# Optimization experiments

Hardware: AMD Instinct MI355X
Metric: run time of the kernel (lower is better)

Reference implementation:

```python
import jax, jax.numpy as jnp
import numpy as np

DELTA_V = 0.1
DELTA_D = 0.5
NUM_LABELS = 33  # label 0 = background, instance ids 1..32


def setup_inputs() -> dict:
    key = jax.random.key(0)
    k1, k2 = jax.random.split(key)
    B, N, D = 8, 131072, 32
    embeddings = jax.random.normal(k1, (B, N, D), dtype=jnp.float32)
    labels = jax.random.randint(k2, (B, N), 0, NUM_LABELS, dtype=jnp.int32)
    return {"embeddings": embeddings, "labels": labels}


def reference(embeddings, labels):
    # embeddings: [B, N, D], labels: [B, N] int (0 = ignore)
    B = embeddings.shape[0]
    dt = embeddings.dtype

    oh = jax.nn.one_hot(labels, NUM_LABELS, dtype=dt)              # [B, N, L]
    counts = oh.sum(1)                                              # [B, L]
    sums = jnp.einsum('bnl,bnd->bld', oh, embeddings)               # [B, L, D]
    means = sums / jnp.maximum(counts, 1.0)[..., None]              # [B, L, D]

    # ---- pull loss: hinge on distance of each point to its instance mean ----
    mean_pt = jnp.take_along_axis(means, labels[..., None], axis=1)  # [B, N, D]
    diff = embeddings - mean_pt
    dist = jnp.sqrt(jnp.sum(diff * diff, -1) + 1e-24)               # [B, N]
    hinge = jnp.maximum(dist - DELTA_V, 0.0)
    seg_mean = jnp.einsum('bnl,bn->bl', oh, hinge) / jnp.maximum(counts, 1.0)  # [B, L]

    present = counts[:, 1:] > 0                                     # [B, L-1]
    n_inst = present.sum(-1).astype(dt)                             # [B]
    pull_b = seg_mean[:, 1:].sum(-1) / (n_inst + 1e-6)
    pull = pull_b.sum() / B

    # ---- push loss: hinge margin between normalized instance means ----
    m = means[:, 1:, :]                                             # [B, L-1, D]
    mn = m / jnp.maximum(jnp.linalg.norm(m, axis=-1, keepdims=True), 1e-12)
    sq = jnp.sum((mn[:, :, None, :] - mn[:, None, :, :]) ** 2, -1)  # [B, K, K]
    dmat = jnp.sqrt(sq + 1e-24)
    K = NUM_LABELS - 1
    triu = jnp.triu(jnp.ones((K, K), dt), 1)
    pmask = triu[None] * present[:, :, None].astype(dt) * present[:, None, :].astype(dt)
    hp = jnp.maximum(2.0 * DELTA_D - dmat, 0.0) * pmask
    push_b = jnp.where(n_inst > 1, hp.sum((-2, -1)) / (pmask.sum((-2, -1)) + 1e-6), 0.0)
    push = push_b.sum() / B

    total = pull + push
    return jnp.stack([total, pull, push])
```

## Files before the change

kernel.cpp:

```cpp
#include <hip/hip_runtime.h>
#include <hip/hip_bf16.h>

#define BATCH 8
#define NPTS  131072
#define DIM   32
#define NLAB  33
#define G1X   128
#define P1PTS 1024
#define BPB2  512

#define OFF_CNT   0
#define OFF_SUM   264
#define OFF_PULL  (264 + 8448)
#define WS_FLOATS (OFF_PULL + 8)

typedef short  bf16x8 __attribute__((ext_vector_type(8)));
typedef float  f32x4  __attribute__((ext_vector_type(4)));

static __device__ __forceinline__ short f2bf(float f) {
  __hip_bfloat16 h = __float2bfloat16(f);
  return *reinterpret_cast<short*>(&h);
}

__global__ __launch_bounds__(256) void pass1_kernel(
    const float* __restrict__ emb, const int* __restrict__ lab,
    float* __restrict__ gsum, float* __restrict__ gcnt) {
  const int b    = blockIdx.y;
  const int tid  = threadIdx.x;
  const int w    = tid >> 6;
  const int lane = tid & 63;

  __shared__ float s_stage[4][32 * 33];
  __shared__ int   s_cnt4[4][NLAB];
  float* st = s_stage[w];

  const size_t base = (size_t)b * NPTS + (size_t)blockIdx.x * P1PTS + w * 256;

  const int m0 = lane & 15;
  const int g  = lane >> 4;
  f32x4 acc[3][2];
#pragma unroll
  for (int t = 0; t < 3; ++t)
#pragma unroll
    for (int u = 0; u < 2; ++u) acc[t][u] = (f32x4){0.f, 0.f, 0.f, 0.f};
  int cnt0 = 0, cnt1 = 0, cnt2 = 0;

  float4 ld[4];
  int labv;
  {
    const float4* src = (const float4*)(emb + base * DIM);
#pragma unroll
    for (int r = 0; r < 4; ++r) ld[r] = src[lane + 64 * r];
    labv = lab[base + (lane & 31)];
  }

  for (int step = 0; step < 8; ++step) {
#pragma unroll
    for (int r = 0; r < 4; ++r) {
      const int i = lane + 64 * r;
      const int p = i >> 3, d0 = (i & 7) * 4;
      st[(d0 + 0) * 33 + p] = ld[r].x;
      st[(d0 + 1) * 33 + p] = ld[r].y;
      st[(d0 + 2) * 33 + p] = ld[r].z;
      st[(d0 + 3) * 33 + p] = ld[r].w;
    }
    const int labv_c = labv;

    if (step < 7) {
      const float4* src = (const float4*)(emb + (base + (step + 1) * 32) * DIM);
#pragma unroll
      for (int r = 0; r < 4; ++r) ld[r] = src[lane + 64 * r];
      labv = lab[base + (step + 1) * 32 + (lane & 31)];
    }

    bf16x8 a0, a1, a2;
#pragma unroll
    for (int j = 0; j < 8; ++j) {
      const int lj = __shfl(labv_c, g * 8 + j);
      const int h0 = (lj == m0), h1 = (lj == m0 + 16), h2 = (lj == m0 + 32);
      a0[j] = h0 ? (short)0x3F80 : (short)0;
      a1[j] = h1 ? (short)0x3F80 : (short)0;
      a2[j] = h2 ? (short)0x3F80 : (short)0;
      cnt0 += h0; cnt1 += h1; cnt2 += h2;
    }

    bf16x8 b0, b1;
#pragma unroll
    for (int j = 0; j < 8; ++j) {
      b0[j] = f2bf(st[m0 * 33 + g * 8 + j]);
      b1[j] = f2bf(st[(m0 + 16) * 33 + g * 8 + j]);
    }

    acc[0][0] = __builtin_amdgcn_mfma_f32_16x16x32_bf16(a0, b0, acc[0][0], 0, 0, 0);
    acc[0][1] = __builtin_amdgcn_mfma_f32_16x16x32_bf16(a0, b1, acc[0][1], 0, 0, 0);
    acc[1][0] = __builtin_amdgcn_mfma_f32_16x16x32_bf16(a1, b0, acc[1][0], 0, 0, 0);
    acc[1][1] = __builtin_amdgcn_mfma_f32_16x16x32_bf16(a1, b1, acc[1][1], 0, 0, 0);
    acc[2][0] = __builtin_amdgcn_mfma_f32_16x16x32_bf16(a2, b0, acc[2][0], 0, 0, 0);
    acc[2][1] = __builtin_amdgcn_mfma_f32_16x16x32_bf16(a2, b1, acc[2][1], 0, 0, 0);
  }

  cnt0 += __shfl_xor(cnt0, 16); cnt0 += __shfl_xor(cnt0, 32);
  cnt1 += __shfl_xor(cnt1, 16); cnt1 += __shfl_xor(cnt1, 32);
  cnt2 += __shfl_xor(cnt2, 16); cnt2 += __shfl_xor(cnt2, 32);
  if (lane < 16)            s_cnt4[w][m0]      = cnt0;
  else if (lane < 32)       s_cnt4[w][m0 + 16] = cnt1;
  if (lane == 32)           s_cnt4[w][32]      = cnt2;

#pragma unroll
  for (int t = 0; t < 2; ++t)
#pragma unroll
    for (int u = 0; u < 2; ++u)
#pragma unroll
      for (int r = 0; r < 4; ++r)
        st[(t * 16 + g * 4 + r) * DIM + m0 + 16 * u] = acc[t][u][r];
  if (lane < 16) {
    st[32 * DIM + m0]      = acc[2][0][0];
    st[32 * DIM + m0 + 16] = acc[2][1][0];
  }
  __syncthreads();

  for (int i = tid; i < NLAB * DIM; i += 256) {
    const float v = s_stage[0][i] + s_stage[1][i] + s_stage[2][i] + s_stage[3][i];
    atomicAdd(&gsum[(size_t)b * (NLAB * DIM) + i], v);
  }
  if (tid < NLAB) {
    const int c = s_cnt4[0][tid] + s_cnt4[1][tid] + s_cnt4[2][tid] + s_cnt4[3][tid];
    atomicAdd(&gcnt[b * NLAB + tid], (float)c);
  }
}

__global__ __launch_bounds__(256) void pass2_kernel(
    const float* __restrict__ emb, const int* __restrict__ lab,
    const float* __restrict__ gsum, const float* __restrict__ gcnt,
    float* __restrict__ pullb) {
  const int b   = blockIdx.y;
  const int tid = threadIdx.x;
  __shared__ __align__(16) float s_mean[NLAB * 36];
  __shared__ float s_w[NLAB];
  __shared__ float s_red[4];

  for (int i = tid; i < NLAB * DIM; i += 256) {
    const int l = i >> 5, d = i & 31;
    const float c = gcnt[b * NLAB + l];
    s_mean[l * 36 + d] = gsum[b * (NLAB * DIM) + i] / fmaxf(c, 1.0f);
  }
  if (tid < 64) {
    const float c = (tid < NLAB) ? gcnt[b * NLAB + tid] : 0.f;
    const int pres = (tid >= 1 && tid < NLAB && c > 0.f) ? 1 : 0;
    const unsigned long long bal = __ballot(pres);
    const float n_inst = (float)__popcll(bal);
    if (tid < NLAB)
      s_w[tid] = pres ? 1.f / (fmaxf(c, 1.f) * (n_inst + 1e-6f)) : 0.f;
  }
  __syncthreads();

  const int sub   = tid >> 3;
  const int lane8 = tid & 7;
  const int d0    = lane8 << 2;
  const size_t base = (size_t)b * NPTS;
  const int p0 = blockIdx.x * 32 + sub;
  constexpr int NIT = NPTS / (BPB2 * 32);

  int labs[NIT];
#pragma unroll
  for (int it = 0; it < NIT; ++it)
    labs[it] = lab[base + p0 + it * (BPB2 * 32)];

  float wacc = 0.f;
#pragma unroll
  for (int it = 0; it < NIT; ++it) {
    const int p = p0 + it * (BPB2 * 32);
    const int l = labs[it];
    const float4 e = *(const float4*)(emb + (base + p) * DIM + d0);
    const float4 m = *(const float4*)(s_mean + l * 36 + d0);
    const float dx = e.x - m.x, dy = e.y - m.y, dz = e.z - m.z, dw = e.w - m.w;
    float s = dx * dx + dy * dy + dz * dz + dw * dw;
    s += __shfl_xor(s, 1);
    s += __shfl_xor(s, 2);
    s += __shfl_xor(s, 4);
    if (lane8 == 0) {
      const float dist = sqrtf(s + 1e-24f);
      wacc += s_w[l] * fmaxf(dist - 0.1f, 0.f);
    }
  }
#pragma unroll
  for (int m = 1; m < 64; m <<= 1) wacc += __shfl_xor(wacc, m);
  if ((tid & 63) == 0) s_red[tid >> 6] = wacc;
  __syncthreads();
  if (tid == 0)
    atomicAdd(&pullb[b], s_red[0] + s_red[1] + s_red[2] + s_red[3]);
}

__global__ __launch_bounds__(512) void finish_kernel(
    const float* __restrict__ gsum, const float* __restrict__ gcnt,
    const float* __restrict__ pullb, float* __restrict__ out) {
  const int tid = threadIdx.x;
  const int b   = tid >> 6;
  const int t   = tid & 63;
  __shared__ __align__(16) float s_mn[BATCH * 32 * DIM];
  __shared__ float s_ps[BATCH];
  float* mn = s_mn + b * 32 * DIM;

  int pres = 0;
  if (t < 32) {
    const int l = t + 1;
    const float cnt = gcnt[b * NLAB + l];
    pres = (cnt > 0.f) ? 1 : 0;
    const float inv = 1.f / fmaxf(cnt, 1.f);
    float v[DIM];
    float n2 = 0.f;
    for (int d = 0; d < DIM; d++) {
      v[d] = gsum[b * (NLAB * DIM) + l * DIM + d] * inv;
      n2  += v[d] * v[d];
    }
    const float scale = 1.f / fmaxf(sqrtf(n2), 1e-12f);
    for (int d = 0; d < DIM; d++) mn[t * DIM + d] = v[d] * scale;
  }
  const unsigned long long bal = __ballot(pres);
  const unsigned int pmask32 = (unsigned int)(bal & 0xFFFFFFFFull);
  const int n_inst = __popc(pmask32);

  __syncthreads();

  float hp_sum = 0.f, pm_sum = 0.f;
  for (int idx = t; idx < 1024; idx += 64) {
    const int i = idx >> 5, j = idx & 31;
    if (j > i && ((pmask32 >> i) & 1u) && ((pmask32 >> j) & 1u)) {
      const float4* a = (const float4*)(mn + i * DIM);
      const float4* c = (const float4*)(mn + j * DIM);
      float sq = 0.f;
      for (int q = 0; q < 8; q++) {
        const float4 av = a[q], cv = c[q];
        const float dx = av.x - cv.x, dy = av.y - cv.y;
        const float dz = av.z - cv.z, dw = av.w - cv.w;
        sq += dx * dx + dy * dy + dz * dz + dw * dw;
      }
      const float dmat = sqrtf(sq + 1e-24f);
      hp_sum += fmaxf(1.0f - dmat, 0.f);
      pm_sum += 1.f;
    }
  }
  for (int m = 1; m < 64; m <<= 1) {
    hp_sum += __shfl_xor(hp_sum, m);
    pm_sum += __shfl_xor(pm_sum, m);
  }
  const float push = (n_inst > 1) ? hp_sum / (pm_sum + 1e-6f) : 0.f;
  if (t == 0) s_ps[b] = push;
  __syncthreads();

  if (tid < 64) {
    float pl = (t < BATCH) ? pullb[t] : 0.f;
    float ps = (t < BATCH) ? s_ps[t] : 0.f;
#pragma unroll
    for (int m = 1; m < 64; m <<= 1) {
      pl += __shfl_xor(pl, m);
      ps += __shfl_xor(ps, m);
    }
    if (t == 0) {
      const float pull_m = pl / (float)BATCH;
      const float push_m = ps / (float)BATCH;
      out[0] = pull_m + push_m;
      out[1] = pull_m;
      out[2] = push_m;
    }
  }
}

extern "C" void kernel_launch(void* const* d_in, const int* in_sizes, int n_in,
                              void* d_out, int out_size, void* d_ws, size_t ws_size,
                              hipStream_t stream) {
  const float* emb = (const float*)d_in[0];
  const int*   lab = (const int*)d_in[1];
  float* out = (float*)d_out;
  float* ws  = (float*)d_ws;

  float* gcnt  = ws + OFF_CNT;
  float* gsum  = ws + OFF_SUM;
  float* pullb = ws + OFF_PULL;

  hipMemsetAsync(d_ws, 0, WS_FLOATS * sizeof(float), stream);

  dim3 grid1(G1X, BATCH);
  dim3 grid2(BPB2, BATCH);
  pass1_kernel<<<grid1, 256, 0, stream>>>(emb, lab, gsum, gcnt);
  pass2_kernel<<<grid2, 256, 0, stream>>>(emb, lab, gsum, gcnt, pullb);
  finish_kernel<<<1, 512, 0, stream>>>(gsum, gcnt, pullb, out);
}
```

Measured before the change: 279.6 us.

## Replace atomic reductions with per-block partials, reduce kernel, and last-block finish

Pass1 now writes per-block partial sums and counts to the workspace, and a separate reduce kernel sums them. This replaces the global float atomics and removes the memset. Pass1 loads embeddings directly from global memory in the layout the MFMA needs instead of staging them through shared memory, and it doubles its grid. The finish kernel is folded into pass2 through a last-block counter, which saves a launch. The cost is an extra reduce launch and about 8.6MB of partial-sum traffic, and the direct pass1 loads are strided rather than coalesced.

```diff
diff --git a/kernel.cpp b/kernel.cpp
--- a/kernel.cpp
+++ b/kernel.cpp
@@ -5,14 +5,15 @@
 #define NPTS  131072
 #define DIM   32
 #define NLAB  33
-#define G1X   128
-#define P1PTS 1024
-#define BPB2  512
-
-#define OFF_CNT   0
-#define OFF_SUM   264
-#define OFF_PULL  (264 + 8448)
-#define WS_FLOATS (OFF_PULL + 8)
+#define B1    256
+#define B2    512
+
+#define OFF_PART  0
+#define OFF_PCNT  (2048 * 1056)
+#define OFF_SUM   (OFF_PCNT + 2048 * 33)
+#define OFF_CNT   (OFF_SUM + 8448)
+#define OFF_PULL  (OFF_CNT + 264)
+#define OFF_CTR   (OFF_PULL + 8)
 
 typedef short  bf16x8 __attribute__((ext_vector_type(8)));
 typedef float  f32x4  __attribute__((ext_vector_type(4)));
@@ -22,22 +23,20 @@
   return *reinterpret_cast<short*>(&h);
 }
 
-__global__ __launch_bounds__(256) void pass1_kernel(
+__global__ __launch_bounds__(256, 6) void pass1_kernel(
     const float* __restrict__ emb, const int* __restrict__ lab,
-    float* __restrict__ gsum, float* __restrict__ gcnt) {
+    float* __restrict__ part, int* __restrict__ pcnt) {
   const int b    = blockIdx.y;
+  const int bx   = blockIdx.x;
   const int tid  = threadIdx.x;
   const int w    = tid >> 6;
   const int lane = tid & 63;
-
-  __shared__ float s_stage[4][32 * 33];
-  __shared__ int   s_cnt4[4][NLAB];
-  float* st = s_stage[w];
-
-  const size_t base = (size_t)b * NPTS + (size_t)blockIdx.x * P1PTS + w * 256;
-
-  const int m0 = lane & 15;
-  const int g  = lane >> 4;
+  const int m0   = lane & 15;
+  const int g    = lane >> 4;
+
+  __shared__ float s_stage[4][NLAB * DIM];
+  __shared__ int   s_cnt[4][NLAB];
+
   f32x4 acc[3][2];
 #pragma unroll
   for (int t = 0; t < 3; ++t)
@@ -45,50 +44,27 @@
     for (int u = 0; u < 2; ++u) acc[t][u] = (f32x4){0.f, 0.f, 0.f, 0.f};
   int cnt0 = 0, cnt1 = 0, cnt2 = 0;
 
-  float4 ld[4];
-  int labv;
-  {
-    const float4* src = (const float4*)(emb + base * DIM);
-#pragma unroll
-    for (int r = 0; r < 4; ++r) ld[r] = src[lane + 64 * r];
-    labv = lab[base + (lane & 31)];
-  }
-
-  for (int step = 0; step < 8; ++step) {
-#pragma unroll
-    for (int r = 0; r < 4; ++r) {
-      const int i = lane + 64 * r;
-      const int p = i >> 3, d0 = (i & 7) * 4;
-      st[(d0 + 0) * 33 + p] = ld[r].x;
-      st[(d0 + 1) * 33 + p] = ld[r].y;
-      st[(d0 + 2) * 33 + p] = ld[r].z;
-      st[(d0 + 3) * 33 + p] = ld[r].w;
-    }
-    const int labv_c = labv;
-
-    if (step < 7) {
-      const float4* src = (const float4*)(emb + (base + (step + 1) * 32) * DIM);
-#pragma unroll
-      for (int r = 0; r < 4; ++r) ld[r] = src[lane + 64 * r];
-      labv = lab[base + (step + 1) * 32 + (lane & 31)];
-    }
-
-    bf16x8 a0, a1, a2;
+  const size_t bbase = (size_t)b * NPTS + (size_t)bx * 512 + w * 128;
+
+#pragma unroll 2
+  for (int s = 0; s < 4; ++s) {
+    const size_t pt = bbase + s * 32;
+    const float* eb = emb + pt * DIM;
+
+    int lj[8];
+#pragma unroll
+    for (int j = 0; j < 8; ++j) lj[j] = lab[pt + g * 8 + j];
+
+    bf16x8 a0, a1, a2, b0, b1;
 #pragma unroll
     for (int j = 0; j < 8; ++j) {
-      const int lj = __shfl(labv_c, g * 8 + j);
-      const int h0 = (lj == m0), h1 = (lj == m0 + 16), h2 = (lj == m0 + 32);
+      b0[j] = f2bf(eb[(g * 8 + j) * DIM + m0]);
+      b1[j] = f2bf(eb[(g * 8 + j) * DIM + m0 + 16]);
+      const int h0 = (lj[j] == m0), h1 = (lj[j] == m0 + 16), h2 = (lj[j] == m0 + 32);
       a0[j] = h0 ? (short)0x3F80 : (short)0;
       a1[j] = h1 ? (short)0x3F80 : (short)0;
       a2[j] = h2 ? (short)0x3F80 : (short)0;
       cnt0 += h0; cnt1 += h1; cnt2 += h2;
-    }
-
-    bf16x8 b0, b1;
-#pragma unroll
-    for (int j = 0; j < 8; ++j) {
-      b0[j] = f2bf(st[m0 * 33 + g * 8 + j]);
-      b1[j] = f2bf(st[(m0 + 16) * 33 + g * 8 + j]);
     }
 
     acc[0][0] = __builtin_amdgcn_mfma_f32_16x16x32_bf16(a0, b0, acc[0][0], 0, 0, 0);
@@ -102,10 +78,11 @@
   cnt0 += __shfl_xor(cnt0, 16); cnt0 += __shfl_xor(cnt0, 32);
   cnt1 += __shfl_xor(cnt1, 16); cnt1 += __shfl_xor(cnt1, 32);
   cnt2 += __shfl_xor(cnt2, 16); cnt2 += __shfl_xor(cnt2, 32);
-  if (lane < 16)            s_cnt4[w][m0]      = cnt0;
-  else if (lane < 32)       s_cnt4[w][m0 + 16] = cnt1;
-  if (lane == 32)           s_cnt4[w][32]      = cnt2;
-
+  if (lane < 16)      s_cnt[w][m0]      = cnt0;
+  else if (lane < 32) s_cnt[w][m0 + 16] = cnt1;
+  if (lane == 32)     s_cnt[w][32]      = cnt2;
+
+  float* st = s_stage[w];
 #pragma unroll
   for (int t = 0; t < 2; ++t)
 #pragma unroll
@@ -119,25 +96,58 @@
   }
   __syncthreads();
 
-  for (int i = tid; i < NLAB * DIM; i += 256) {
-    const float v = s_stage[0][i] + s_stage[1][i] + s_stage[2][i] + s_stage[3][i];
-    atomicAdd(&gsum[(size_t)b * (NLAB * DIM) + i], v);
-  }
-  if (tid < NLAB) {
-    const int c = s_cnt4[0][tid] + s_cnt4[1][tid] + s_cnt4[2][tid] + s_cnt4[3][tid];
-    atomicAdd(&gcnt[b * NLAB + tid], (float)c);
+  const int blk = b * B1 + bx;
+  for (int i = tid; i < NLAB * DIM; i += 256)
+    part[(size_t)blk * (NLAB * DIM) + i] =
+        s_stage[0][i] + s_stage[1][i] + s_stage[2][i] + s_stage[3][i];
+  if (tid < NLAB)
+    pcnt[blk * NLAB + tid] =
+        s_cnt[0][tid] + s_cnt[1][tid] + s_cnt[2][tid] + s_cnt[3][tid];
+}
+
+__global__ __launch_bounds__(256) void reduce_kernel(
+    const float* __restrict__ part, const int* __restrict__ pcnt,
+    float* __restrict__ gsum, float* __restrict__ gcnt,
+    float* __restrict__ pullb, unsigned* __restrict__ ctr) {
+  const int o = blockIdx.x * 256 + threadIdx.x;
+  {
+    const int b = o / (NLAB * DIM), r = o % (NLAB * DIM);
+    float s = 0.f;
+    const float* p = part + (size_t)(b * B1) * (NLAB * DIM) + r;
+#pragma unroll 8
+    for (int k = 0; k < B1; ++k) s += p[(size_t)k * (NLAB * DIM)];
+    gsum[o] = s;
+  }
+
+  if (blockIdx.x == 0) {
+    const int tid = threadIdx.x;
+    for (int t = tid; t < BATCH * NLAB; t += 256) {
+      const int bb = t / NLAB, l = t % NLAB;
+      int c = 0;
+      const int* q = pcnt + bb * B1 * NLAB + l;
+#pragma unroll 8
+      for (int k = 0; k < B1; ++k) c += q[k * NLAB];
+      gcnt[t] = (float)c;
+    }
+    if (tid < BATCH) pullb[tid] = 0.f;
+    if (tid == BATCH) *ctr = 0u;
   }
 }
 
 __global__ __launch_bounds__(256) void pass2_kernel(
     const float* __restrict__ emb, const int* __restrict__ lab,
     const float* __restrict__ gsum, const float* __restrict__ gcnt,
-    float* __restrict__ pullb) {
+    float* __restrict__ pullb, unsigned* __restrict__ ctr,
+    float* __restrict__ out) {
   const int b   = blockIdx.y;
   const int tid = threadIdx.x;
   __shared__ __align__(16) float s_mean[NLAB * 36];
   __shared__ float s_w[NLAB];
   __shared__ float s_red[4];
+  __shared__ __align__(16) float s_mn[32 * DIM];
+  __shared__ int   s_pres[32];
+  __shared__ float s_hp[4], s_pm[4], s_ps[BATCH];
+  __shared__ int   s_islast;
 
   for (int i = tid; i < NLAB * DIM; i += 256) {
     const int l = i >> 5, d = i & 31;
@@ -159,17 +169,17 @@
   const int d0    = lane8 << 2;
   const size_t base = (size_t)b * NPTS;
   const int p0 = blockIdx.x * 32 + sub;
-  constexpr int NIT = NPTS / (BPB2 * 32);
+  constexpr int NIT = NPTS / (B2 * 32);
 
   int labs[NIT];
 #pragma unroll
   for (int it = 0; it < NIT; ++it)
-    labs[it] = lab[base + p0 + it * (BPB2 * 32)];
+    labs[it] = lab[base + p0 + it * (B2 * 32)];
 
   float wacc = 0.f;
 #pragma unroll
   for (int it = 0; it < NIT; ++it) {
-    const int p = p0 + it * (BPB2 * 32);
+    const int p = p0 + it * (B2 * 32);
     const int l = labs[it];
     const float4 e = *(const float4*)(emb + (base + p) * DIM + d0);
     const float4 m = *(const float4*)(s_mean + l * 36 + d0);
@@ -187,70 +197,78 @@
   for (int m = 1; m < 64; m <<= 1) wacc += __shfl_xor(wacc, m);
   if ((tid & 63) == 0) s_red[tid >> 6] = wacc;
   __syncthreads();
-  if (tid == 0)
+  if (tid == 0) {
     atomicAdd(&pullb[b], s_red[0] + s_red[1] + s_red[2] + s_red[3]);
-}
-
-__global__ __launch_bounds__(512) void finish_kernel(
-    const float* __restrict__ gsum, const float* __restrict__ gcnt,
-    const float* __restrict__ pullb, float* __restrict__ out) {
-  const int tid = threadIdx.x;
-  const int b   = tid >> 6;
-  const int t   = tid & 63;
-  __shared__ __align__(16) float s_mn[BATCH * 32 * DIM];
-  __shared__ float s_ps[BATCH];
-  float* mn = s_mn + b * 32 * DIM;
-
-  int pres = 0;
-  if (t < 32) {
-    const int l = t + 1;
-    const float cnt = gcnt[b * NLAB + l];
-    pres = (cnt > 0.f) ? 1 : 0;
+    __threadfence();
+    const unsigned v = atomicAdd(ctr, 1u);
+    s_islast = (v == (unsigned)(B2 * BATCH - 1)) ? 1 : 0;
+  }
+  __syncthreads();
+  if (!s_islast) return;
+
+  __threadfence();
+  const int fl  = tid >> 3;
+  const int fs  = tid & 7;
+
+  for (int bb = 0; bb < BATCH; ++bb) {
+    const float cnt = gcnt[bb * NLAB + fl + 1];
+    float4 v = *(const float4*)(gsum + (size_t)(bb * NLAB + fl + 1) * DIM + fs * 4);
     const float inv = 1.f / fmaxf(cnt, 1.f);
-    float v[DIM];
-    float n2 = 0.f;
-    for (int d = 0; d < DIM; d++) {
-      v[d] = gsum[b * (NLAB * DIM) + l * DIM + d] * inv;
-      n2  += v[d] * v[d];
-    }
+    v.x *= inv; v.y *= inv; v.z *= inv; v.w *= inv;
+    float n2 = v.x * v.x + v.y * v.y + v.z * v.z + v.w * v.w;
+    n2 += __shfl_xor(n2, 1);
+    n2 += __shfl_xor(n2, 2);
+    n2 += __shfl_xor(n2, 4);
     const float scale = 1.f / fmaxf(sqrtf(n2), 1e-12f);
-    for (int d = 0; d < DIM; d++) mn[t * DIM + d] = v[d] * scale;
-  }
-  const unsigned long long bal = __ballot(pres);
-  const unsigned int pmask32 = (unsigned int)(bal & 0xFFFFFFFFull);
-  const int n_inst = __popc(pmask32);
-
-  __syncthreads();
-
-  float hp_sum = 0.f, pm_sum = 0.f;
-  for (int idx = t; idx < 1024; idx += 64) {
-    const int i = idx >> 5, j = idx & 31;
-    if (j > i && ((pmask32 >> i) & 1u) && ((pmask32 >> j) & 1u)) {
-      const float4* a = (const float4*)(mn + i * DIM);
-      const float4* c = (const float4*)(mn + j * DIM);
-      float sq = 0.f;
-      for (int q = 0; q < 8; q++) {
-        const float4 av = a[q], cv = c[q];
-        const float dx = av.x - cv.x, dy = av.y - cv.y;
-        const float dz = av.z - cv.z, dw = av.w - cv.w;
-        sq += dx * dx + dy * dy + dz * dz + dw * dw;
+    v.x *= scale; v.y *= scale; v.z *= scale; v.w *= scale;
+    *(float4*)(s_mn + fl * DIM + fs * 4) = v;
+    if (fs == 0) s_pres[fl] = (cnt > 0.f) ? 1 : 0;
+    if (tid < 4) { s_hp[tid] = 0.f; s_pm[tid] = 0.f; }
+    __syncthreads();
+
+    float hp = 0.f, pm = 0.f;
+    for (int idx = tid; idx < 1024; idx += 256) {
+      const int i = idx >> 5, j = idx & 31;
+      if (j > i && s_pres[i] && s_pres[j]) {
+        const float4* a = (const float4*)(s_mn + i * DIM);
+        const float4* c = (const float4*)(s_mn + j * DIM);
+        float sq = 0.f;
+#pragma unroll
+        for (int q = 0; q < 8; ++q) {
+          const float4 av = a[q], cv = c[q];
+          const float ddx = av.x - cv.x, ddy = av.y - cv.y;
+          const float ddz = av.z - cv.z, ddw = av.w - cv.w;
+          sq += ddx * ddx + ddy * ddy + ddz * ddz + ddw * ddw;
+        }
+        const float dmat = sqrtf(sq + 1e-24f);
+        hp += fmaxf(1.0f - dmat, 0.f);
+        pm += 1.f;
       }
-      const float dmat = sqrtf(sq + 1e-24f);
-      hp_sum += fmaxf(1.0f - dmat, 0.f);
-      pm_sum += 1.f;
-    }
-  }
-  for (int m = 1; m < 64; m <<= 1) {
-    hp_sum += __shfl_xor(hp_sum, m);
-    pm_sum += __shfl_xor(pm_sum, m);
-  }
-  const float push = (n_inst > 1) ? hp_sum / (pm_sum + 1e-6f) : 0.f;
-  if (t == 0) s_ps[b] = push;
-  __syncthreads();
+    }
+#pragma unroll
+    for (int m = 1; m < 64; m <<= 1) {
+      hp += __shfl_xor(hp, m);
+      pm += __shfl_xor(pm, m);
+    }
+    if ((tid & 63) == 0) { s_hp[tid >> 6] = hp; s_pm[tid >> 6] = pm; }
+    __syncthreads();
+    if (tid == 0) {
+      int ni = 0;
+      for (int i = 0; i < 32; ++i) ni += s_pres[i];
+      const float hpt = s_hp[0] + s_hp[1] + s_hp[2] + s_hp[3];
+      const float pmt = s_pm[0] + s_pm[1] + s_pm[2] + s_pm[3];
+      s_ps[bb] = (ni > 1) ? hpt / (pmt + 1e-6f) : 0.f;
+    }
+    __syncthreads();
+  }
 
   if (tid < 64) {
-    float pl = (t < BATCH) ? pullb[t] : 0.f;
-    float ps = (t < BATCH) ? s_ps[t] : 0.f;
+    const int t = tid;
+    float pl = 0.f, ps = 0.f;
+    if (t < BATCH) {
+      pl = atomicAdd(&pullb[t], 0.f);
+      ps = s_ps[t];
+    }
 #pragma unroll
     for (int m = 1; m < 64; m <<= 1) {
       pl += __shfl_xor(pl, m);
@@ -274,15 +292,15 @@
   float* out = (float*)d_out;
   float* ws  = (float*)d_ws;
 
-  float* gcnt  = ws + OFF_CNT;
-  float* gsum  = ws + OFF_SUM;
-  float* pullb = ws + OFF_PULL;
-
-  hipMemsetAsync(d_ws, 0, WS_FLOATS * sizeof(float), stream);
-
-  dim3 grid1(G1X, BATCH);
-  dim3 grid2(BPB2, BATCH);
-  pass1_kernel<<<grid1, 256, 0, stream>>>(emb, lab, gsum, gcnt);
-  pass2_kernel<<<grid2, 256, 0, stream>>>(emb, lab, gsum, gcnt, pullb);
-  finish_kernel<<<1, 512, 0, stream>>>(gsum, gcnt, pullb, out);
-}
+  float*    part  = ws + OFF_PART;
+  int*      pcnt  = (int*)(ws + OFF_PCNT);
+  float*    gsum  = ws + OFF_SUM;
+  float*    gcnt  = ws + OFF_CNT;
+  float*    pullb = ws + OFF_PULL;
+  unsigned* ctr   = (unsigned*)(ws + OFF_CTR);
+
+  pass1_kernel<<<dim3(B1, BATCH), 256, 0, stream>>>(emb, lab, part, pcnt);
+  reduce_kernel<<<33, 256, 0, stream>>>(part, pcnt, gsum, gcnt, pullb, ctr);
+  pass2_kernel<<<dim3(B2, BATCH), 256, 0, stream>>>(emb, lab, gsum, gcnt,
+                                                    pullb, ctr, out);
+}
```

Measured after the change: 385.6 us. 1.38x slower.
